# Kernel optimization log

Hardware: AMD Instinct MI355X
Metric: run time of the kernel (lower is better)

The kernel has to match this reference:

```python
import jax, jax.numpy as jnp
import numpy as np

EMBED_DIM = 1024
HEADS = 16
HEAD_DIM = EMBED_DIM // HEADS
SEQ = 2048
N_BATCH = 4


def setup_inputs() -> dict:
    key = jax.random.key(0)
    ks = jax.random.split(key, 9)
    s = 1.0 / np.sqrt(HEAD_DIM)
    so = 1.0 / np.sqrt(EMBED_DIM)
    return {
        "values": jax.random.normal(ks[0], (SEQ, N_BATCH, EMBED_DIM), jnp.float32),
        "keys": jax.random.normal(ks[1], (SEQ, N_BATCH, EMBED_DIM), jnp.float32),
        "queries": jax.random.normal(ks[2], (SEQ, N_BATCH, EMBED_DIM), jnp.float32),
        "src_mask": jax.random.randint(ks[3], (N_BATCH, 1, 1, SEQ), 0, 2, jnp.int32),
        "Wv": jax.random.uniform(ks[4], (HEAD_DIM, HEAD_DIM), jnp.float32, -s, s),
        "Wk": jax.random.uniform(ks[5], (HEAD_DIM, HEAD_DIM), jnp.float32, -s, s),
        "Wq": jax.random.uniform(ks[6], (HEAD_DIM, HEAD_DIM), jnp.float32, -s, s),
        "Wo": jax.random.uniform(ks[7], (EMBED_DIM, EMBED_DIM), jnp.float32, -so, so),
        "bo": jax.random.uniform(ks[8], (EMBED_DIM,), jnp.float32, -so, so),
    }


def reference(values, keys, queries, src_mask, Wv, Wk, Wq, Wo, bo):
    N = queries.shape[1]
    Lv, Lk, Lq = values.shape[0], keys.shape[0], queries.shape[0]
    # Faithful to the original (buggy) reshape of (L, N, E) -> (N, L, H, D)
    v = values.reshape(N, Lv, HEADS, HEAD_DIM) @ Wv.T
    k = keys.reshape(N, Lk, HEADS, HEAD_DIM) @ Wk.T
    q = queries.reshape(N, Lq, HEADS, HEAD_DIM) @ Wq.T
    energy = jnp.einsum("nqhd,nkhd->nhqk", q, k)  # (N, H, Q, K)
    energy = jnp.where(src_mask == 0, jnp.float32(-1e20), energy)
    attn = jax.nn.softmax(energy / jnp.sqrt(jnp.float32(EMBED_DIM)), axis=3)
    out = jnp.einsum("nhql,nlhd->nqhd", attn, v).reshape(Lq, N, EMBED_DIM)
    return out @ Wo.T + bo
```

## Files before the change

### kernel.cpp

```cpp
#include <hip/hip_runtime.h>
#include <hip/hip_bf16.h>
#include <stdint.h>
#include <string.h>

#define EMBED 1024
#define HEADS 16
#define HD    64
#define SEQ   2048
#define NB    4
#define ROWS  (SEQ * NB)
#define NH    (NB * HEADS)

typedef __attribute__((ext_vector_type(8)))  short short8;
typedef __attribute__((ext_vector_type(4)))  float f32x4;
typedef __attribute__((ext_vector_type(16))) float f32x16;
typedef __attribute__((ext_vector_type(4)))  unsigned short u16x4;

#define MFMA16(a, b, c) __builtin_amdgcn_mfma_f32_16x16x32_bf16((a), (b), (c), 0, 0, 0)
#define MFMA32(a, b, c) __builtin_amdgcn_mfma_f32_32x32x16_bf16((a), (b), (c), 0, 0, 0)

__device__ inline unsigned short f2b(float f) {
    unsigned u = __builtin_bit_cast(unsigned, f);
    u += 0x7fffu + ((u >> 16) & 1u);
    return (unsigned short)(u >> 16);
}

__device__ inline unsigned pkhu(float a, float b) {
    unsigned ua = __builtin_bit_cast(unsigned, a) + 0x8000u;
    unsigned ub = __builtin_bit_cast(unsigned, b) + 0x8000u;
    return (ua >> 16) | (ub & 0xffff0000u);
}

#define EXP2(x) __builtin_amdgcn_exp2f(x)

__device__ inline short8 ld8(const unsigned short* p) {
    return *reinterpret_cast<const short8*>(p);
}

__global__ __launch_bounds__(256) void cvt_bf16_kernel(const float* __restrict__ in,
                                                       unsigned short* __restrict__ out,
                                                       int nelem) {
    int i = (blockIdx.x * 256 + threadIdx.x) * 4;
    if (i + 3 < nelem) {
        float4 v = *reinterpret_cast<const float4*>(in + i);
        u16x4 o;
        o[0] = f2b(v.x); o[1] = f2b(v.y); o[2] = f2b(v.z); o[3] = f2b(v.w);
        *reinterpret_cast<u16x4*>(out + i) = o;
    }
}

__global__ __launch_bounds__(64) void maskbits_kernel(const int* __restrict__ mask,
                                                      unsigned* __restrict__ mb) {
    int w = blockIdx.x * 64 + threadIdx.x;
    unsigned v = 0;
#pragma unroll
    for (int j = 0; j < 32; ++j)
        v |= (mask[w * 32 + j] != 0 ? 1u : 0u) << j;
    mb[w] = v;
}

__global__ __launch_bounds__(64) void proj_kernel(const float* __restrict__ X,
                                                  const float* __restrict__ W,
                                                  unsigned short* __restrict__ out) {
    const int lane = threadIdx.x;
    const int lo = lane & 15, hi = lane >> 4;
    const int r0 = blockIdx.x * 16;
    const int h  = blockIdx.y;

    short8 a[2];
#pragma unroll
    for (int s = 0; s < 2; ++s) {
        const float4* src = reinterpret_cast<const float4*>(
            X + (size_t)(r0 + lo) * EMBED + h * HD + s * 32 + hi * 8);
        float4 v0 = src[0], v1 = src[1];
        short8 t;
        t[0] = (short)f2b(v0.x); t[1] = (short)f2b(v0.y);
        t[2] = (short)f2b(v0.z); t[3] = (short)f2b(v0.w);
        t[4] = (short)f2b(v1.x); t[5] = (short)f2b(v1.y);
        t[6] = (short)f2b(v1.z); t[7] = (short)f2b(v1.w);
        a[s] = t;
    }
    short8 b[4][2];
#pragma unroll
    for (int u = 0; u < 4; ++u)
#pragma unroll
        for (int s = 0; s < 2; ++s) {
            const float4* src = reinterpret_cast<const float4*>(
                W + (size_t)(16 * u + lo) * HD + s * 32 + hi * 8);
            float4 v0 = src[0], v1 = src[1];
            short8 t;
            t[0] = (short)f2b(v0.x); t[1] = (short)f2b(v0.y);
            t[2] = (short)f2b(v0.z); t[3] = (short)f2b(v0.w);
            t[4] = (short)f2b(v1.x); t[5] = (short)f2b(v1.y);
            t[6] = (short)f2b(v1.z); t[7] = (short)f2b(v1.w);
            b[u][s] = t;
        }

    f32x4 acc[4] = {};
#pragma unroll
    for (int u = 0; u < 4; ++u)
#pragma unroll
        for (int s = 0; s < 2; ++s)
            acc[u] = MFMA16(a[s], b[u][s], acc[u]);

    const int n  = r0 >> 11;
    const int l0 = r0 & (SEQ - 1);
    const size_t nh = (size_t)(n * HEADS + h);
#pragma unroll
    for (int u = 0; u < 4; ++u)
#pragma unroll
        for (int r = 0; r < 4; ++r)
            out[nh * (SEQ * HD) + (size_t)(l0 + hi * 4 + r) * HD + 16 * u + lo] =
                f2b(acc[u][r]);
}

__global__ __launch_bounds__(256) void projv_kernel(const float* __restrict__ X,
                                                    const float* __restrict__ W,
                                                    unsigned short* __restrict__ out) {
    const int tid = threadIdx.x;
    const int w = tid >> 6, lane = tid & 63;
    const int lo = lane & 15, hi = lane >> 4;
    const int r0 = blockIdx.x * 64;
    const int rw = r0 + w * 16;
    const int h  = blockIdx.y;

    __shared__ unsigned short T[64 * 73];

    short8 a[2];
#pragma unroll
    for (int s = 0; s < 2; ++s) {
        const float4* src = reinterpret_cast<const float4*>(
            X + (size_t)(rw + lo) * EMBED + h * HD + s * 32 + hi * 8);
        float4 v0 = src[0], v1 = src[1];
        short8 t;
        t[0] = (short)f2b(v0.x); t[1] = (short)f2b(v0.y);
        t[2] = (short)f2b(v0.z); t[3] = (short)f2b(v0.w);
        t[4] = (short)f2b(v1.x); t[5] = (short)f2b(v1.y);
        t[6] = (short)f2b(v1.z); t[7] = (short)f2b(v1.w);
        a[s] = t;
    }
    short8 b[4][2];
#pragma unroll
    for (int u = 0; u < 4; ++u)
#pragma unroll
        for (int s = 0; s < 2; ++s) {
            const float4* src = reinterpret_cast<const float4*>(
                W + (size_t)(16 * u + lo) * HD + s * 32 + hi * 8);
            float4 v0 = src[0], v1 = src[1];
            short8 t;
            t[0] = (short)f2b(v0.x); t[1] = (short)f2b(v0.y);
            t[2] = (short)f2b(v0.z); t[3] = (short)f2b(v0.w);
            t[4] = (short)f2b(v1.x); t[5] = (short)f2b(v1.y);
            t[6] = (short)f2b(v1.z); t[7] = (short)f2b(v1.w);
            b[u][s] = t;
        }

    f32x4 acc[4] = {};
#pragma unroll
    for (int u = 0; u < 4; ++u)
#pragma unroll
        for (int s = 0; s < 2; ++s)
            acc[u] = MFMA16(a[s], b[u][s], acc[u]);

#pragma unroll
    for (int u = 0; u < 4; ++u)
#pragma unroll
        for (int r = 0; r < 4; ++r)
            T[(w * 16 + hi * 4 + r) * 73 + 16 * u + lo] = f2b(acc[u][r]);
    __syncthreads();

    const int d = tid >> 2, lc = (tid & 3) * 16;
    const int n = r0 >> 11, l0 = r0 & (SEQ - 1);
    union { unsigned short s[16]; uint4 v[2]; } pk;
#pragma unroll
    for (int j = 0; j < 16; ++j) pk.s[j] = T[(lc + j) * 73 + d];
    unsigned short* dst = out + (size_t)(n * HEADS + h) * (HD * SEQ)
                              + (size_t)d * SEQ + l0 + lc;
    *reinterpret_cast<uint4*>(dst)     = pk.v[0];
    *reinterpret_cast<uint4*>(dst + 8) = pk.v[1];
}

#define KST 72
#define VST 40

__global__ __launch_bounds__(128, 2) void attn_kernel(const unsigned short* __restrict__ Qb,
                                                      const unsigned short* __restrict__ Kb,
                                                      const unsigned short* __restrict__ Vt,
                                                      const unsigned* __restrict__ mbits,
                                                      unsigned short* __restrict__ Aout) {
    const int tid  = threadIdx.x;
    const int w    = tid >> 6;
    const int lane = tid & 63;
    const int lo = lane & 31, hi = lane >> 5;
    const int nhidx = blockIdx.y;
    const int n = nhidx >> 4, h = nhidx & 15;
    const int q0 = blockIdx.x * 128 + w * 64;

    const unsigned short* Qp = Qb + (size_t)nhidx * SEQ * HD;
    const unsigned short* Kp = Kb + (size_t)nhidx * SEQ * HD;
    const unsigned short* Vp = Vt + (size_t)nhidx * HD * SEQ;
    const unsigned* mb = mbits + n * (SEQ / 32);

    __shared__ __align__(16) unsigned short Klds[2][32 * KST];
    __shared__ __align__(16) unsigned short Vlds[2][64 * VST];

    const int kr = (tid * 2) >> 3, kb0 = ((tid * 2) & 7) * 8;
    const int vr = (tid * 2) >> 2, vb0 = ((tid * 2) & 3) * 8;

    uint4 stK0, stK1, stV0, stV1;
#define LOADSTAGE(KB_)                                                        \
    {                                                                         \
        const unsigned short* kp_ = Kp + (size_t)((KB_) + kr) * HD + kb0;     \
        const unsigned short* vp_ = Vp + (size_t)vr * SEQ + (KB_) + vb0;      \
        stK0 = *reinterpret_cast<const uint4*>(kp_);                          \
        stK1 = *reinterpret_cast<const uint4*>(kp_ + 8);                      \
        stV0 = *reinterpret_cast<const uint4*>(vp_);                          \
        stV1 = *reinterpret_cast<const uint4*>(vp_ + 8);                      \
    }
#define WRITESTAGE(BUF)                                                       \
    {                                                                         \
        *reinterpret_cast<uint4*>(&Klds[BUF][kr * KST + kb0])     = stK0;     \
        *reinterpret_cast<uint4*>(&Klds[BUF][kr * KST + kb0 + 8]) = stK1;     \
        *reinterpret_cast<uint4*>(&Vlds[BUF][vr * VST + vb0])     = stV0;     \
        *reinterpret_cast<uint4*>(&Vlds[BUF][vr * VST + vb0 + 8]) = stV1;     \
    }

    short8 qfA[4], qfB[4];
#pragma unroll
    for (int s = 0; s < 4; ++s) {
        qfA[s] = ld8(Qp + (size_t)(q0 + lo) * HD + s * 16 + hi * 8);
        qfB[s] = ld8(Qp + (size_t)(q0 + 32 + lo) * HD + s * 16 + hi * 8);
    }

    f32x16 o0A = {}, o1A = {}, o0B = {}, o1B = {};
    float lsumA = 0.0f, lsumB = 0.0f;

    const float KS    = 0.045084220027780106f;
    const float M0    = 8.0f;
    const float TMASK = -4.5e18f;

    LOADSTAGE(0)

    int cur = 0;
    for (int kt = 0; kt < SEQ / 32; ++kt) {
        WRITESTAGE(cur)
        if (kt + 1 < SEQ / 32) LOADSTAGE((kt + 1) * 32)
        __syncthreads();

        const unsigned short* Kl = Klds[cur];
        const unsigned short* Vl = Vlds[cur];

        f32x16 saA = {}, saB = {};
#pragma unroll
        for (int s = 0; s < 4; ++s) {
            short8 kf = *reinterpret_cast<const short8*>(Kl + lo * KST + s * 16 + hi * 8);
            saA = MFMA32(kf, qfA[s], saA);
            saB = MFMA32(kf, qfB[s], saB);
        }

        short8 vf[2][2];
#pragma unroll
        for (int dt = 0; dt < 2; ++dt)
#pragma unroll
            for (int s = 0; s < 2; ++s) {
                const unsigned short* vp = Vl + (32 * dt + lo) * VST + s * 16;
                uint2 c0 = *reinterpret_cast<const uint2*>(vp + 4 * hi);
                uint2 c1 = *reinterpret_cast<const uint2*>(vp + 12 - 4 * hi);
                union { short8 s8; unsigned u[4]; } uu;
                uu.u[0] = c0.x; uu.u[1] = c0.y; uu.u[2] = c1.x; uu.u[3] = c1.y;
                vf[dt][s] = uu.s8;
            }

        unsigned mw = mb[kt] >> (4 * hi);
        float pA[16], pB[16];
#pragma unroll
        for (int r = 0; r < 16; ++r) {
            const int bp = (r & 3) + 8 * (r >> 2);
            const bool keep = (mw >> bp) & 1u;
            float ta = fmaf(saA[r], KS, -M0);
            float tb = fmaf(saB[r], KS, -M0);
            float ea = EXP2(keep ? ta : TMASK);
            float eb = EXP2(keep ? tb : TMASK);
            pA[r] = ea; lsumA += ea;
            pB[r] = eb; lsumB += eb;
        }

#define PACK_PB(P, PB_)                                                       \
        {                                                                     \
            unsigned W0[4], W1[4];                                            \
            _Pragma("unroll") for (int g = 0; g < 4; ++g) {                   \
                W0[g] = pkhu(P[4 * g],     P[4 * g + 1]);                     \
                W1[g] = pkhu(P[4 * g + 2], P[4 * g + 3]);                     \
            }                                                                 \
            _Pragma("unroll") for (int s2 = 0; s2 < 2; ++s2) {                \
                unsigned sw0 = (unsigned)__shfl_xor((int)W0[2 * s2 + 1], 32); \
                unsigned sw1 = (unsigned)__shfl_xor((int)W1[2 * s2 + 1], 32); \
                union { short8 s8; unsigned u[4]; } uu;                       \
                uu.u[0] = W0[2 * s2]; uu.u[1] = W1[2 * s2];                   \
                uu.u[2] = sw0;        uu.u[3] = sw1;                          \
                (PB_)[s2] = uu.s8;                                            \
            }                                                                 \
        }
        short8 pbA[2], pbB[2];
        PACK_PB(pA, pbA)
        PACK_PB(pB, pbB)
#undef PACK_PB

#pragma unroll
        for (int s = 0; s < 2; ++s) {
            o0A = MFMA32(vf[0][s], pbA[s], o0A);
            o1A = MFMA32(vf[1][s], pbA[s], o1A);
            o0B = MFMA32(vf[0][s], pbB[s], o0B);
            o1B = MFMA32(vf[1][s], pbB[s], o1B);
        }

        __syncthreads();
        cur ^= 1;
    }

    float lA = lsumA + __shfl_xor(lsumA, 32);
    float lB = lsumB + __shfl_xor(lsumB, 32);

    float invA = 1.0f / lA;
    float invB = 1.0f / lB;
    const size_t rbA = (size_t)(n * SEQ + q0 + lo) * EMBED + h * HD;
    const size_t rbB = (size_t)(n * SEQ + q0 + 32 + lo) * EMBED + h * HD;
#pragma unroll
    for (int r = 0; r < 16; ++r) {
        int dl = (r & 3) + 8 * (r >> 2) + 4 * hi;
        Aout[rbA + dl]      = f2b(o0A[r] * invA);
        Aout[rbA + 32 + dl] = f2b(o1A[r] * invA);
        Aout[rbB + dl]      = f2b(o0B[r] * invB);
        Aout[rbB + 32 + dl] = f2b(o1B[r] * invB);
    }
#undef LOADSTAGE
#undef WRITESTAGE
}

#define OST 40
__global__ __launch_bounds__(256, 2) void outproj_kernel(const unsigned short* __restrict__ A,
                                                         const unsigned short* __restrict__ Wob,
                                                         const float* __restrict__ bo,
                                                         float* __restrict__ Y) {
    const int tid  = threadIdx.x;
    const int w    = tid >> 6;
    const int lane = tid & 63;
    const int lo = lane & 15, hi = lane >> 4;
    const int r0 = blockIdx.x * 128;
    const int c0 = blockIdx.y * 128;

    __shared__ __align__(16) unsigned short Al[128 * OST];
    __shared__ __align__(16) unsigned short Bl[128 * OST];

    const int srow = tid >> 2, scb = (tid & 3) * 8;
    uint4 sA0, sA1, sB0, sB1;
#define OLOAD(K_)                                                             \
    {                                                                         \
        sA0 = *reinterpret_cast<const uint4*>(A + (size_t)(r0 + srow) * EMBED + (K_) + scb);        \
        sA1 = *reinterpret_cast<const uint4*>(A + (size_t)(r0 + 64 + srow) * EMBED + (K_) + scb);   \
        sB0 = *reinterpret_cast<const uint4*>(Wob + (size_t)(c0 + srow) * EMBED + (K_) + scb);      \
        sB1 = *reinterpret_cast<const uint4*>(Wob + (size_t)(c0 + 64 + srow) * EMBED + (K_) + scb); \
    }
#define OWRITE()                                                              \
    {                                                                         \
        *reinterpret_cast<uint4*>(&Al[srow * OST + scb])        = sA0;        \
        *reinterpret_cast<uint4*>(&Al[(64 + srow) * OST + scb]) = sA1;        \
        *reinterpret_cast<uint4*>(&Bl[srow * OST + scb])        = sB0;        \
        *reinterpret_cast<uint4*>(&Bl[(64 + srow) * OST + scb]) = sB1;        \
    }

    f32x4 acc[2][8] = {};
    OLOAD(0)
    for (int kt = 0; kt < EMBED / 32; ++kt) {
        OWRITE()
        if (kt + 1 < EMBED / 32) OLOAD((kt + 1) * 32)
        __syncthreads();

        short8 a0 = ld8(&Al[(w * 32 + lo) * OST + hi * 8]);
        short8 a1 = ld8(&Al[(w * 32 + 16 + lo) * OST + hi * 8]);
#pragma unroll
        for (int u = 0; u < 8; ++u) {
            short8 b = ld8(&Bl[(u * 16 + lo) * OST + hi * 8]);
            acc[0][u] = MFMA16(a0, b, acc[0][u]);
            acc[1][u] = MFMA16(a1, b, acc[1][u]);
        }
        __syncthreads();
    }

#pragma unroll
    for (int mi = 0; mi < 2; ++mi)
#pragma unroll
        for (int u = 0; u < 8; ++u) {
            int e = c0 + u * 16 + lo;
            float bv = bo[e];
#pragma unroll
            for (int r = 0; r < 4; ++r)
                Y[(size_t)(r0 + w * 32 + mi * 16 + hi * 4 + r) * EMBED + e] =
                    acc[mi][u][r] + bv;
        }
#undef OLOAD
#undef OWRITE
}

extern "C" void kernel_launch(void* const* d_in, const int* in_sizes, int n_in,
                              void* d_out, int out_size, void* d_ws, size_t ws_size,
                              hipStream_t stream) {
    const float* values  = (const float*)d_in[0];
    const float* keys    = (const float*)d_in[1];
    const float* queries = (const float*)d_in[2];
    const int*   mask    = (const int*)d_in[3];
    const float* Wv = (const float*)d_in[4];
    const float* Wk = (const float*)d_in[5];
    const float* Wq = (const float*)d_in[6];
    const float* Wo = (const float*)d_in[7];
    const float* bo = (const float*)d_in[8];
    float* Y = (float*)d_out;

    const size_t QKV     = (size_t)NH * SEQ * HD * sizeof(unsigned short);
    const size_t ABYTES  = (size_t)ROWS * EMBED * sizeof(unsigned short);
    const size_t WOBYTES = (size_t)EMBED * EMBED * sizeof(unsigned short);
    const size_t MBYTES  = (size_t)NB * (SEQ / 32) * sizeof(unsigned);
    if (ws_size < 3 * QKV + ABYTES + WOBYTES + MBYTES) return;

    char* ws = (char*)d_ws;
    unsigned short* Qb  = (unsigned short*)(ws);
    unsigned short* Kb  = (unsigned short*)(ws + QKV);
    unsigned short* Vt  = (unsigned short*)(ws + 2 * QKV);
    unsigned short* Ab  = (unsigned short*)(ws + 3 * QKV);
    unsigned short* Wob = (unsigned short*)(ws + 3 * QKV + ABYTES);
    unsigned*       Mb  = (unsigned*)(ws + 3 * QKV + ABYTES + WOBYTES);

    cvt_bf16_kernel<<<dim3(EMBED * EMBED / (256 * 4)), 256, 0, stream>>>(Wo, Wob, EMBED * EMBED);
    maskbits_kernel<<<dim3(4), 64, 0, stream>>>(mask, Mb);
    proj_kernel<<<dim3(ROWS / 16, HEADS), 64, 0, stream>>>(queries, Wq, Qb);
    proj_kernel<<<dim3(ROWS / 16, HEADS), 64, 0, stream>>>(keys,    Wk, Kb);
    projv_kernel<<<dim3(ROWS / 64, HEADS), 256, 0, stream>>>(values, Wv, Vt);
    attn_kernel<<<dim3(SEQ / 128, NH), 128, 0, stream>>>(Qb, Kb, Vt, Mb, Ab);
    outproj_kernel<<<dim3(ROWS / 128, EMBED / 128), 256, 0, stream>>>(Ab, Wob, bo, Y);
}
```

Baseline: 203.0 us.

## Swizzle attention block order and widen out-projection tile to 128x256

The attention kernel remaps its linear block index with a stride-8 swizzle, so concurrently running blocks come from different (batch, head) pairs and query tiles, which spreads L2/XCD locality differently. The out-projection now uses 512-thread blocks covering 128 rows by 256 columns, each wave owning a 16-row strip across 16 column tiles. This halves how often A tiles are reloaded and halves the grid, at the cost of one A fragment reused across 16 MFMAs, more LDS, and fewer blocks in flight.

```diff
diff --git a/kernel.cpp b/kernel.cpp
--- a/kernel.cpp
+++ b/kernel.cpp
@@ -192,9 +192,14 @@
     const int w    = tid >> 6;
     const int lane = tid & 63;
     const int lo = lane & 31, hi = lane >> 5;
-    const int nhidx = blockIdx.y;
+
+    const int bid = blockIdx.y * 16 + blockIdx.x;
+    const int swz = (bid & 7) * 128 + (bid >> 3);
+    const int qb_i  = swz & 15;
+    const int nhidx = swz >> 4;
+
     const int n = nhidx >> 4, h = nhidx & 15;
-    const int q0 = blockIdx.x * 128 + w * 64;
+    const int q0 = qb_i * 128 + w * 64;
 
     const unsigned short* Qp = Qb + (size_t)nhidx * SEQ * HD;
     const unsigned short* Kp = Kb + (size_t)nhidx * SEQ * HD;
@@ -338,7 +343,7 @@
 }
 
 #define OST 40
-__global__ __launch_bounds__(256, 2) void outproj_kernel(const unsigned short* __restrict__ A,
+__global__ __launch_bounds__(512, 2) void outproj_kernel(const unsigned short* __restrict__ A,
                                                          const unsigned short* __restrict__ Wob,
                                                          const float* __restrict__ bo,
                                                          float* __restrict__ Y) {
@@ -347,57 +352,53 @@
     const int lane = tid & 63;
     const int lo = lane & 15, hi = lane >> 4;
     const int r0 = blockIdx.x * 128;
-    const int c0 = blockIdx.y * 128;
+    const int c0 = blockIdx.y * 256;
 
     __shared__ __align__(16) unsigned short Al[128 * OST];
-    __shared__ __align__(16) unsigned short Bl[128 * OST];
-
-    const int srow = tid >> 2, scb = (tid & 3) * 8;
-    uint4 sA0, sA1, sB0, sB1;
+    __shared__ __align__(16) unsigned short Bl[256 * OST];
+
+    const int arow = tid >> 2, acb = (tid & 3) * 8;
+    const int brow = tid >> 1, bcb = (tid & 1) * 16;
+
+    uint4 sA, sB0, sB1;
 #define OLOAD(K_)                                                             \
     {                                                                         \
-        sA0 = *reinterpret_cast<const uint4*>(A + (size_t)(r0 + srow) * EMBED + (K_) + scb);        \
-        sA1 = *reinterpret_cast<const uint4*>(A + (size_t)(r0 + 64 + srow) * EMBED + (K_) + scb);   \
-        sB0 = *reinterpret_cast<const uint4*>(Wob + (size_t)(c0 + srow) * EMBED + (K_) + scb);      \
-        sB1 = *reinterpret_cast<const uint4*>(Wob + (size_t)(c0 + 64 + srow) * EMBED + (K_) + scb); \
+        sA  = *reinterpret_cast<const uint4*>(A + (size_t)(r0 + arow) * EMBED + (K_) + acb);       \
+        const unsigned short* bp_ = Wob + (size_t)(c0 + brow) * EMBED + (K_) + bcb;                \
+        sB0 = *reinterpret_cast<const uint4*>(bp_);                           \
+        sB1 = *reinterpret_cast<const uint4*>(bp_ + 8);                       \
     }
 #define OWRITE()                                                              \
     {                                                                         \
-        *reinterpret_cast<uint4*>(&Al[srow * OST + scb])        = sA0;        \
-        *reinterpret_cast<uint4*>(&Al[(64 + srow) * OST + scb]) = sA1;        \
-        *reinterpret_cast<uint4*>(&Bl[srow * OST + scb])        = sB0;        \
-        *reinterpret_cast<uint4*>(&Bl[(64 + srow) * OST + scb]) = sB1;        \
-    }
-
-    f32x4 acc[2][8] = {};
+        *reinterpret_cast<uint4*>(&Al[arow * OST + acb])     = sA;            \
+        *reinterpret_cast<uint4*>(&Bl[brow * OST + bcb])     = sB0;           \
+        *reinterpret_cast<uint4*>(&Bl[brow * OST + bcb + 8]) = sB1;           \
+    }
+
+    f32x4 acc[16] = {};
     OLOAD(0)
     for (int kt = 0; kt < EMBED / 32; ++kt) {
         OWRITE()
         if (kt + 1 < EMBED / 32) OLOAD((kt + 1) * 32)
         __syncthreads();
 
-        short8 a0 = ld8(&Al[(w * 32 + lo) * OST + hi * 8]);
-        short8 a1 = ld8(&Al[(w * 32 + 16 + lo) * OST + hi * 8]);
-#pragma unroll
-        for (int u = 0; u < 8; ++u) {
+        short8 a = ld8(&Al[(w * 16 + lo) * OST + hi * 8]);
+#pragma unroll
+        for (int u = 0; u < 16; ++u) {
             short8 b = ld8(&Bl[(u * 16 + lo) * OST + hi * 8]);
-            acc[0][u] = MFMA16(a0, b, acc[0][u]);
-            acc[1][u] = MFMA16(a1, b, acc[1][u]);
+            acc[u] = MFMA16(a, b, acc[u]);
         }
         __syncthreads();
     }
 
 #pragma unroll
-    for (int mi = 0; mi < 2; ++mi)
-#pragma unroll
-        for (int u = 0; u < 8; ++u) {
-            int e = c0 + u * 16 + lo;
-            float bv = bo[e];
-#pragma unroll
-            for (int r = 0; r < 4; ++r)
-                Y[(size_t)(r0 + w * 32 + mi * 16 + hi * 4 + r) * EMBED + e] =
-                    acc[mi][u][r] + bv;
-        }
+    for (int u = 0; u < 16; ++u) {
+        int e = c0 + u * 16 + lo;
+        float bv = bo[e];
+#pragma unroll
+        for (int r = 0; r < 4; ++r)
+            Y[(size_t)(r0 + w * 16 + hi * 4 + r) * EMBED + e] = acc[u][r] + bv;
+    }
 #undef OLOAD
 #undef OWRITE
 }
@@ -436,5 +437,5 @@
     proj_kernel<<<dim3(ROWS / 16, HEADS), 64, 0, stream>>>(keys,    Wk, Kb);
     projv_kernel<<<dim3(ROWS / 64, HEADS), 256, 0, stream>>>(values, Wv, Vt);
     attn_kernel<<<dim3(SEQ / 128, NH), 128, 0, stream>>>(Qb, Kb, Vt, Mb, Ab);
-    outproj_kernel<<<dim3(ROWS / 128, EMBED / 128), 256, 0, stream>>>(Ab, Wob, bo, Y);
-}
+    outproj_kernel<<<dim3(ROWS / 128, EMBED / 256), 512, 0, stream>>>(Ab, Wob, bo, Y);
+}
```

Result: slower. 212.4 us (+4.6%).
